# Kernel tuning notes

Hardware: AMD Instinct MI355X
Metric: run time of the kernel (lower is better)

The kernel has to match this reference:

```python
import jax, jax.numpy as jnp
import numpy as np

L, H, E, D, FF, V, CTX = 8, 16, 1024, 64, 4096, 2048, 2048
B, T = 4, 1024


def _ln(x, g, b, eps=1e-5):
    mu = x.mean(-1, keepdims=True)
    var = ((x - mu) ** 2).mean(-1, keepdims=True)
    return (x - mu) * jax.lax.rsqrt(var + eps) * g + b


def setup_inputs() -> dict:
    key = jax.random.key(0)
    ks = jax.random.split(key, 12)
    s = 0.02
    return {
        "tokens": jax.random.randint(ks[0], (B, T), 0, V),
        "tok_emb": jax.random.normal(ks[1], (V, E), jnp.float32) * s,
        "pos_emb": jax.random.normal(ks[2], (CTX, E), jnp.float32) * s,
        "Wq": jax.random.normal(ks[3], (L, H, E, D), jnp.float32) * s,
        "Wk": jax.random.normal(ks[4], (L, H, E, D), jnp.float32) * s,
        "Wv": jax.random.normal(ks[5], (L, H, E, D), jnp.float32) * s,
        "Wo": jax.random.normal(ks[6], (L, H * D, E), jnp.float32) * s,
        "bo": jnp.zeros((L, E), jnp.float32),
        "ln1_g": jnp.ones((L, E), jnp.float32),
        "ln1_b": jnp.zeros((L, E), jnp.float32),
        "ln2_g": jnp.ones((L, E), jnp.float32),
        "ln2_b": jnp.zeros((L, E), jnp.float32),
        "W1": jax.random.normal(ks[7], (L, E, FF), jnp.float32) * s,
        "b1": jnp.zeros((L, FF), jnp.float32),
        "W2": jax.random.normal(ks[8], (L, FF, E), jnp.float32) * s,
        "b2": jnp.zeros((L, E), jnp.float32),
        "lnf_g": jnp.ones((E,), jnp.float32),
        "lnf_b": jnp.zeros((E,), jnp.float32),
        "Wlm": jax.random.normal(ks[9], (E, V), jnp.float32) * s,
        "blm": jnp.zeros((V,), jnp.float32),
    }


def reference(tokens, tok_emb, pos_emb, Wq, Wk, Wv, Wo, bo, ln1_g, ln1_b,
              ln2_g, ln2_b, W1, b1, W2, b2, lnf_g, lnf_b, Wlm, blm):
    # NOTE: original indexes pos_embd with token ids (pos_embd(x.int()))
    x = tok_emb[tokens] + pos_emb[tokens]  # [B,T,E]
    t = x.shape[1]
    causal = jnp.tril(jnp.ones((t, t), bool))
    scale = 1.0 / jnp.sqrt(jnp.float32(D))
    for l in range(L):
        x = _ln(x, ln1_g[l], ln1_b[l])
        q = jnp.einsum('bte,hed->bhtd', x, Wq[l])
        k = jnp.einsum('bte,hed->bhtd', x, Wk[l])
        v = jnp.einsum('bte,hed->bhtd', x, Wv[l])
        scores = jnp.einsum('bhtd,bhsd->bhts', q, k) * scale
        scores = jnp.where(causal, scores, -jnp.inf)
        att = jax.nn.softmax(scores, axis=-1)
        o = jnp.einsum('bhts,bhsd->bhtd', att, v)
        o = o.transpose(0, 2, 1, 3).reshape(x.shape[0], t, H * D)
        x = x + o @ Wo[l] + bo[l]
        x = _ln(x, ln2_g[l], ln2_b[l])
        x = x + jax.nn.relu(x @ W1[l] + b1[l]) @ W2[l] + b2[l]
    x = _ln(x, lnf_g, lnf_b)
    return x @ Wlm + blm
```

## Files before the change

kernel.cpp:

```cpp
#include <hip/hip_runtime.h>
#include <hip/hip_bf16.h>

#define LAYERS 8
#define H_ 16
#define E_ 1024
#define D_ 64
#define FF_ 4096
#define V_ 2048
#define B_ 4
#define T_ 1024
#define MTOK (B_*T_)

typedef __bf16 bf16x8_t __attribute__((ext_vector_type(8)));
typedef __bf16 bf16x4_t __attribute__((ext_vector_type(4)));
typedef float f32x4_t __attribute__((ext_vector_type(4)));
typedef __hip_bfloat16 bf16_t;

__device__ __forceinline__ bf16_t f2b(float f) { return __float2bfloat16(f); }

__global__ void embed_kernel(const int* __restrict__ tokens,
                             const float* __restrict__ te,
                             const float* __restrict__ pe,
                             bf16_t* __restrict__ x) {
  int row = blockIdx.x;
  int tok = tokens[row];
  int t = threadIdx.x;
  float4 va = ((const float4*)(te + (size_t)tok * E_))[t];
  float4 vp = ((const float4*)(pe + (size_t)tok * E_))[t];
  bf16x4_t o;
  o[0] = (__bf16)(va.x + vp.x); o[1] = (__bf16)(va.y + vp.y);
  o[2] = (__bf16)(va.z + vp.z); o[3] = (__bf16)(va.w + vp.w);
  ((bf16x4_t*)(x + (size_t)row * E_))[t] = o;
}

__global__ __launch_bounds__(256) void ln_kernel(const bf16_t* __restrict__ xin,
                                                 bf16_t* __restrict__ xout,
                                                 const float* __restrict__ g,
                                                 const float* __restrict__ b) {
  int row = blockIdx.x, tid = threadIdx.x;
  bf16x4_t v4 = ((const bf16x4_t*)(xin + (size_t)row * E_))[tid];
  float v0 = (float)v4[0], v1 = (float)v4[1], v2 = (float)v4[2], v3 = (float)v4[3];
  float s  = v0 + v1 + v2 + v3;
  float sq = v0*v0 + v1*v1 + v2*v2 + v3*v3;
  for (int off = 32; off; off >>= 1) {
    s  += __shfl_xor(s, off, 64);
    sq += __shfl_xor(sq, off, 64);
  }
  __shared__ float2 wred[4];
  if ((tid & 63) == 0) wred[tid >> 6] = make_float2(s, sq);
  __syncthreads();
  float2 w0 = wred[0], w1 = wred[1], w2 = wred[2], w3 = wred[3];
  float S = w0.x + w1.x + w2.x + w3.x, SQ = w0.y + w1.y + w2.y + w3.y;
  float mean = S * (1.0f / E_);
  float var  = SQ * (1.0f / E_) - mean * mean;
  float inv = rsqrtf(var + 1e-5f);
  float4 gv = ((const float4*)g)[tid];
  float4 bv = ((const float4*)b)[tid];
  bf16x4_t o;
  o[0] = (__bf16)((v0 - mean) * inv * gv.x + bv.x);
  o[1] = (__bf16)((v1 - mean) * inv * gv.y + bv.y);
  o[2] = (__bf16)((v2 - mean) * inv * gv.z + bv.z);
  o[3] = (__bf16)((v3 - mean) * inv * gv.w + bv.w);
  ((bf16x4_t*)(xout + (size_t)row * E_))[tid] = o;
}

__global__ void transpose_kernel(const float* __restrict__ in, bf16_t* __restrict__ out,
                                 int R, int C) {
  __shared__ float tile[32][33];
  int z = blockIdx.z;
  const float* ib = in + (size_t)z * R * C;
  bf16_t* ob = out + (size_t)z * R * C;
  int r0 = blockIdx.y * 32, c0 = blockIdx.x * 32;
  int tx = threadIdx.x, ty = threadIdx.y;
  for (int i = 0; i < 4; i++)
    tile[ty + i * 8][tx] = ib[(size_t)(r0 + ty + i * 8) * C + (c0 + tx)];
  __syncthreads();
  for (int i = 0; i < 4; i++)
    ob[(size_t)(c0 + ty + i * 8) * R + (r0 + tx)] = f2b(tile[tx][ty + i * 8]);
}

enum { MODE_F32 = 0, MODE_BF16 = 1, MODE_QKV = 2 };

__device__ __forceinline__ void gload16(const bf16_t* g, bf16_t* l) {
  __builtin_amdgcn_global_load_lds((const __attribute__((address_space(1))) void*)g,
                                   (__attribute__((address_space(3))) void*)l, 16, 0, 0);
}

__device__ __forceinline__ int xcd_swz(int flat, int nwg) {
  int q = nwg >> 3, r = nwg & 7;
  int xcd = flat & 7, idx = flat >> 3;
  return (xcd < r ? xcd * (q + 1) : r * (q + 1) + (xcd - r) * q) + idx;
}

template <int MODE>
__global__ __launch_bounds__(512) void gemm3_kernel(
    const bf16_t* __restrict__ A, int lda,
    const bf16_t* __restrict__ Bt, int ldb,
    void* __restrict__ C, long long sCz,
    const float* __restrict__ bias,
    int M, int N, int kspan, int relu) {
  constexpr int ABUFE = 256 * 64;
  constexpr int BBUFE = 128 * 64;
  __shared__ __align__(16) bf16_t LA[3 * ABUFE];
  __shared__ __align__(16) bf16_t LB[3 * BBUFE];
  int tid = threadIdx.x, lane = tid & 63, wave = tid >> 6;
  int wm = wave >> 1, wn = wave & 1;
  int z = blockIdx.z;
  int nwg = gridDim.x * gridDim.y;
  int flat = xcd_swz(blockIdx.y * gridDim.x + blockIdx.x, nwg);
  int m0 = (flat / gridDim.x) * 256, n0 = (flat % gridDim.x) * 128;
  const bf16_t* Ab = A + (size_t)m0 * lda + (size_t)z * kspan;
  const bf16_t* Bb = Bt + (size_t)n0 * ldb + (size_t)z * kspan;
  int sr = lane & 15, sc = (lane >> 4) * 8;

  f32x4_t acc[4][4];
#pragma unroll
  for (int i = 0; i < 4; i++)
#pragma unroll
    for (int j = 0; j < 4; j++)
      acc[i][j] = (f32x4_t){0.f, 0.f, 0.f, 0.f};

  auto stageh = [&](int b, int kt, int h) {
    int kg = kt * 64;
#pragma unroll
    for (int ch = 0; ch < 2; ch++) {
      int sub = wave * 4 + 2 * h + ch;
      gload16(Ab + (size_t)((sub >> 1) * 16 + sr) * lda + kg + (sub & 1) * 32 + sc,
              LA + b * ABUFE + sub * 512);
    }
    {
      int sub = wave * 2 + h;
      gload16(Bb + (size_t)((sub >> 1) * 16 + sr) * ldb + kg + (sub & 1) * 32 + sc,
              LB + b * BBUFE + sub * 512);
    }
  };

  auto phase = [&](int b, int ks, int t, int nk) {
    bf16x8_t af[4], bfv[4];
    unsigned abase = (unsigned)(size_t)(LA + b * ABUFE);
    unsigned bbase = (unsigned)(size_t)(LB + b * BBUFE);
#pragma unroll
    for (int i = 0; i < 4; i++) {
      unsigned ad = abase + (unsigned)((((wm * 4 + i) * 2 + ks) * 512 + lane * 8) * 2);
      asm volatile("ds_read_b128 %0, %1" : "=v"(af[i]) : "v"(ad));
    }
#pragma unroll
    for (int j = 0; j < 4; j++) {
      unsigned bd = bbase + (unsigned)((((wn * 4 + j) * 2 + ks) * 512 + lane * 8) * 2);
      asm volatile("ds_read_b128 %0, %1" : "=v"(bfv[j]) : "v"(bd));
    }
    if (t + 2 < nk) stageh((t + 2) % 3, t + 2, ks);
    __builtin_amdgcn_s_barrier();
    asm volatile("s_waitcnt lgkmcnt(0)" ::: "memory");
    __builtin_amdgcn_sched_barrier(0);
    __builtin_amdgcn_s_setprio(1);
#pragma unroll
    for (int i = 0; i < 4; i++)
#pragma unroll
      for (int j = 0; j < 4; j++)
        acc[i][j] = __builtin_amdgcn_mfma_f32_16x16x32_bf16(af[i], bfv[j], acc[i][j], 0, 0, 0);
    __builtin_amdgcn_s_setprio(0);
  };

  int nk = kspan / 64;
  stageh(0, 0, 0); stageh(0, 0, 1);
  stageh(1, 1, 0); stageh(1, 1, 1);
  for (int t = 0; t < nk; ++t) {
    int b = t % 3;
    if (t + 1 < nk) { asm volatile("s_waitcnt vmcnt(6)" ::: "memory"); }
    else            { asm volatile("s_waitcnt vmcnt(0)" ::: "memory"); }
    __builtin_amdgcn_s_barrier();
    phase(b, 0, t, nk);
    phase(b, 1, t, nk);
  }

#pragma unroll
  for (int i = 0; i < 4; i++)
#pragma unroll
    for (int j = 0; j < 4; j++) {
      f32x4_t v = acc[i][j];
      int n = n0 + wn * 64 + j * 16 + (lane & 15);
      int mb = m0 + wm * 64 + i * 16 + (lane >> 4) * 4;
#pragma unroll
      for (int r = 0; r < 4; r++) {
        int m = mb + r;
        float val = v[r];
        if (bias) val += bias[n];
        if (relu) val = fmaxf(val, 0.f);
        if (MODE == MODE_F32) {
          size_t idx = (size_t)z * sCz + (size_t)m * N + n;
          ((float*)C)[idx] = val;
        } else if (MODE == MODE_BF16) {
          size_t idx = (size_t)z * sCz + (size_t)m * N + n;
          ((bf16_t*)C)[idx] = f2b(val);
        } else {
          int sect = n >> 10, hd = n & 1023, h = hd >> 6, d = hd & 63;
          int b2 = m >> 10, tt = m & 1023;
          size_t base = (size_t)sect * ((size_t)B_ * H_ * T_ * D_);
          size_t idx = base + ((size_t)(b2 * H_ + h) << 16) +
                       (sect == 2 ? (size_t)((d << 10) + tt) : (size_t)((tt << 6) + d));
          ((bf16_t*)C)[idx] = f2b(val);
        }
      }
    }
}

template <int NS>
__global__ __launch_bounds__(256) void splitk_reduce_kernel(const bf16_t* __restrict__ p,
                                                            const bf16_t* __restrict__ t,
                                                            bf16_t* __restrict__ r,
                                                            const float* __restrict__ bias) {
  size_t i = (size_t)blockIdx.x * 256 + threadIdx.x;
  bf16x8_t tv = ((const bf16x8_t*)t)[i];
  int base = (int)((i * 8) & (E_ - 1));
  float acc[8];
#pragma unroll
  for (int j = 0; j < 8; j++) acc[j] = (float)tv[j] + bias[base + j];
#pragma unroll
  for (int s = 0; s < NS; s++) {
    bf16x8_t pv = ((const bf16x8_t*)p)[i + (size_t)s * ((size_t)MTOK * E_ / 8)];
#pragma unroll
    for (int j = 0; j < 8; j++) acc[j] += (float)pv[j];
  }
  bf16x8_t ov;
#pragma unroll
  for (int j = 0; j < 8; j++) ov[j] = (__bf16)acc[j];
  ((bf16x8_t*)r)[i] = ov;
}

#define KPAD 72

__global__ __launch_bounds__(256) void flash_kernel(
    const bf16_t* __restrict__ q,
    const bf16_t* __restrict__ kk,
    const bf16_t* __restrict__ vt,
    bf16_t* __restrict__ o) {
  __shared__ __align__(16) bf16_t Ks[64 * KPAD];
  __shared__ __align__(16) bf16_t Vs[64 * KPAD];
  __shared__ __align__(16) bf16_t Ps[4][16 * KPAD];
  int bid = blockIdx.x;
  int qi = 15 - (bid >> 6);
  int bh = bid & 63;
  int b = bh >> 4, h = bh & 15;
  const bf16_t* qb = q + ((size_t)bh << 16);
  const bf16_t* kb = kk + ((size_t)bh << 16);
  const bf16_t* vb = vt + ((size_t)bh << 16);
  int tid = threadIdx.x, lane = tid & 63, wave = tid >> 6;
  int lr = lane & 15, lg = lane >> 4;
  int qbase = qi * 64;

  bf16x8_t qf[2];
  {
    const bf16_t* qrow = qb + (size_t)(qbase + wave * 16 + lr) * D_ + lg * 8;
    qf[0] = *(const bf16x8_t*)(qrow);
    qf[1] = *(const bf16x8_t*)(qrow + 32);
  }

  float m_r[4], l_r[4];
  f32x4_t oc[4];
#pragma unroll
  for (int r = 0; r < 4; r++) { m_r[r] = -1e30f; l_r[r] = 0.f; }
#pragma unroll
  for (int j = 0; j < 4; j++) oc[j] = (f32x4_t){0.f, 0.f, 0.f, 0.f};

  int srow = tid >> 2, scol = (tid & 3) * 16;

  bf16x8_t k0, k1, v0, v1;
  {
    const bf16_t* kg = kb + (size_t)srow * D_ + scol;
    k0 = *(const bf16x8_t*)kg;
    k1 = *(const bf16x8_t*)(kg + 8);
    const bf16_t* vg = vb + (size_t)srow * T_ + scol;
    v0 = *(const bf16x8_t*)vg;
    v1 = *(const bf16x8_t*)(vg + 8);
  }

  for (int s = 0; s <= qi; s++) {
    __syncthreads();
    *(bf16x8_t*)(&Ks[srow * KPAD + scol]) = k0;
    *(bf16x8_t*)(&Ks[srow * KPAD + scol + 8]) = k1;
    *(bf16x8_t*)(&Vs[srow * KPAD + scol]) = v0;
    *(bf16x8_t*)(&Vs[srow * KPAD + scol + 8]) = v1;
    __syncthreads();

    if (s < qi) {
      int kv1 = (s + 1) * 64;
      const bf16_t* kg = kb + (size_t)(kv1 + srow) * D_ + scol;
      k0 = *(const bf16x8_t*)kg;
      k1 = *(const bf16x8_t*)(kg + 8);
      const bf16_t* vg = vb + (size_t)srow * T_ + kv1 + scol;
      v0 = *(const bf16x8_t*)vg;
      v1 = *(const bf16x8_t*)(vg + 8);
    }

    int kv0 = s * 64;
    f32x4_t sc[4];
#pragma unroll
    for (int j = 0; j < 4; j++) {
      f32x4_t a = (f32x4_t){0.f, 0.f, 0.f, 0.f};
      bf16x8_t b0 = *(const bf16x8_t*)(&Ks[(j * 16 + lr) * KPAD + lg * 8]);
      bf16x8_t b1 = *(const bf16x8_t*)(&Ks[(j * 16 + lr) * KPAD + lg * 8 + 32]);
      a = __builtin_amdgcn_mfma_f32_16x16x32_bf16(qf[0], b0, a, 0, 0, 0);
      a = __builtin_amdgcn_mfma_f32_16x16x32_bf16(qf[1], b1, a, 0, 0, 0);
      sc[j] = a;
    }
    if (s == qi) {
#pragma unroll
      for (int j = 0; j < 4; j++)
#pragma unroll
        for (int r = 0; r < 4; r++) {
          int kvp = kv0 + j * 16 + lr;
          int qp  = qbase + wave * 16 + lg * 4 + r;
          sc[j][r] = (kvp <= qp) ? sc[j][r] * 0.125f : -1e30f;
        }
    } else {
#pragma unroll
      for (int j = 0; j < 4; j++)
#pragma unroll
        for (int r = 0; r < 4; r++) sc[j][r] *= 0.125f;
    }

    float ex[4];
#pragma unroll
    for (int r = 0; r < 4; r++) {
      float v = fmaxf(fmaxf(sc[0][r], sc[1][r]), fmaxf(sc[2][r], sc[3][r]));
      v = fmaxf(v, __shfl_xor(v, 1, 64));
      v = fmaxf(v, __shfl_xor(v, 2, 64));
      v = fmaxf(v, __shfl_xor(v, 4, 64));
      v = fmaxf(v, __shfl_xor(v, 8, 64));
      float mn = fmaxf(m_r[r], v);
      ex[r] = __expf(m_r[r] - mn);
      m_r[r] = mn;
      l_r[r] *= ex[r];
    }
#pragma unroll
    for (int j = 0; j < 4; j++)
#pragma unroll
      for (int r = 0; r < 4; r++) {
        float p = __expf(sc[j][r] - m_r[r]);
        l_r[r] += p;
        Ps[wave][(lg * 4 + r) * KPAD + j * 16 + lr] = f2b(p);
      }

#pragma unroll
    for (int j = 0; j < 4; j++)
#pragma unroll
      for (int r = 0; r < 4; r++) oc[j][r] *= ex[r];

    bf16x8_t pa0 = *(const bf16x8_t*)(&Ps[wave][lr * KPAD + lg * 8]);
    bf16x8_t pa1 = *(const bf16x8_t*)(&Ps[wave][lr * KPAD + lg * 8 + 32]);
#pragma unroll
    for (int j = 0; j < 4; j++) {
      bf16x8_t vb0 = *(const bf16x8_t*)(&Vs[(j * 16 + lr) * KPAD + lg * 8]);
      bf16x8_t vb1 = *(const bf16x8_t*)(&Vs[(j * 16 + lr) * KPAD + lg * 8 + 32]);
      oc[j] = __builtin_amdgcn_mfma_f32_16x16x32_bf16(pa0, vb0, oc[j], 0, 0, 0);
      oc[j] = __builtin_amdgcn_mfma_f32_16x16x32_bf16(pa1, vb1, oc[j], 0, 0, 0);
    }
  }

#pragma unroll
  for (int r = 0; r < 4; r++) {
    float v = l_r[r];
    v += __shfl_xor(v, 1, 64);
    v += __shfl_xor(v, 2, 64);
    v += __shfl_xor(v, 4, 64);
    v += __shfl_xor(v, 8, 64);
    l_r[r] = 1.f / v;
  }
  bf16_t* ob = o + ((size_t)(b * T_ + qbase + wave * 16)) * (H_ * D_) + h * D_;
#pragma unroll
  for (int j = 0; j < 4; j++)
#pragma unroll
    for (int r = 0; r < 4; r++) {
      int qrow = lg * 4 + r;
      ob[(size_t)qrow * (H_ * D_) + j * 16 + lr] = f2b(oc[j][r] * l_r[r]);
    }
}

extern "C" void kernel_launch(void* const* d_in, const int* in_sizes, int n_in,
                              void* d_out, int out_size, void* d_ws, size_t ws_size,
                              hipStream_t stream) {
  (void)in_sizes; (void)n_in; (void)out_size; (void)ws_size;
  const int*   tokens = (const int*)d_in[0];
  const float* tok_emb = (const float*)d_in[1];
  const float* pos_emb = (const float*)d_in[2];
  const float* Wq = (const float*)d_in[3];
  const float* Wk = (const float*)d_in[4];
  const float* Wv = (const float*)d_in[5];
  const float* Wo = (const float*)d_in[6];
  const float* bo = (const float*)d_in[7];
  const float* ln1_g = (const float*)d_in[8];
  const float* ln1_b = (const float*)d_in[9];
  const float* ln2_g = (const float*)d_in[10];
  const float* ln2_b = (const float*)d_in[11];
  const float* W1 = (const float*)d_in[12];
  const float* b1 = (const float*)d_in[13];
  const float* W2 = (const float*)d_in[14];
  const float* b2 = (const float*)d_in[15];
  const float* lnf_g = (const float*)d_in[16];
  const float* lnf_b = (const float*)d_in[17];
  const float* Wlm = (const float*)d_in[18];
  const float* blm = (const float*)d_in[19];

  char* w = (char*)d_ws;
  size_t off = 0;
  auto alloc = [&](size_t bytes) { void* p = (void*)(w + off); off += (bytes + 255) & ~(size_t)255; return p; };
  bf16_t* r    = (bf16_t*)alloc((size_t)MTOK * E_ * 2);
  bf16_t* t    = (bf16_t*)alloc((size_t)MTOK * E_ * 2);
  bf16_t* q    = (bf16_t*)alloc((size_t)B_ * H_ * T_ * D_ * 2);
  bf16_t* kk   = (bf16_t*)alloc((size_t)B_ * H_ * T_ * D_ * 2);
  bf16_t* vt   = (bf16_t*)alloc((size_t)B_ * H_ * T_ * D_ * 2);
  bf16_t* o    = (bf16_t*)alloc((size_t)MTOK * E_ * 2);
  bf16_t* h1   = (bf16_t*)alloc((size_t)MTOK * FF_ * 2);
  bf16_t* WqkvT = (bf16_t*)alloc((size_t)3 * E_ * H_ * D_ * 2);
  bf16_t* WoT  = (bf16_t*)alloc((size_t)E_ * H_ * D_ * 2);
  bf16_t* W1T  = (bf16_t*)alloc((size_t)E_ * FF_ * 2);
  bf16_t* W2T  = (bf16_t*)alloc((size_t)E_ * FF_ * 2);
  bf16_t* WlmT = (bf16_t*)alloc((size_t)E_ * V_ * 2);
  bf16_t* p2   = (bf16_t*)alloc((size_t)2 * MTOK * E_ * 2);

  embed_kernel<<<MTOK, 256, 0, stream>>>(tokens, tok_emb, pos_emb, r);
  transpose_kernel<<<dim3(V_ / 32, E_ / 32, 1), dim3(32, 8), 0, stream>>>(Wlm, WlmT, E_, V_);

  for (int l = 0; l < LAYERS; l++) {
    ln_kernel<<<MTOK, 256, 0, stream>>>(r, t, ln1_g + l * E_, ln1_b + l * E_);

    transpose_kernel<<<dim3(D_ / 32, E_ / 32, H_), dim3(32, 8), 0, stream>>>(
        Wq + (size_t)l * H_ * E_ * D_, WqkvT, E_, D_);
    transpose_kernel<<<dim3(D_ / 32, E_ / 32, H_), dim3(32, 8), 0, stream>>>(
        Wk + (size_t)l * H_ * E_ * D_, WqkvT + (size_t)E_ * H_ * D_, E_, D_);
    transpose_kernel<<<dim3(D_ / 32, E_ / 32, H_), dim3(32, 8), 0, stream>>>(
        Wv + (size_t)l * H_ * E_ * D_, WqkvT + (size_t)2 * E_ * H_ * D_, E_, D_);
    transpose_kernel<<<dim3(E_ / 32, (H_ * D_) / 32, 1), dim3(32, 8), 0, stream>>>(
        Wo + (size_t)l * H_ * D_ * E_, WoT, H_ * D_, E_);
    transpose_kernel<<<dim3(FF_ / 32, E_ / 32, 1), dim3(32, 8), 0, stream>>>(
        W1 + (size_t)l * E_ * FF_, W1T, E_, FF_);
    transpose_kernel<<<dim3(E_ / 32, FF_ / 32, 1), dim3(32, 8), 0, stream>>>(
        W2 + (size_t)l * FF_ * E_, W2T, FF_, E_);

    gemm3_kernel<MODE_QKV><<<dim3(24, 16, 1), 512, 0, stream>>>(
        t, E_, WqkvT, E_, q, 0, nullptr, MTOK, 3 * H_ * D_, E_, 0);

    flash_kernel<<<1024, 256, 0, stream>>>(q, kk, vt, o);

    gemm3_kernel<MODE_BF16><<<dim3(8, 16, 2), 512, 0, stream>>>(
        o, H_ * D_, WoT, H_ * D_, p2, (long long)MTOK * E_, nullptr,
        MTOK, E_, (H_ * D_) / 2, 0);
    splitk_reduce_kernel<2><<<MTOK * E_ / 2048, 256, 0, stream>>>(p2, t, r, bo + l * E_);

    ln_kernel<<<MTOK, 256, 0, stream>>>(r, t, ln2_g + l * E_, ln2_b + l * E_);

    gemm3_kernel<MODE_BF16><<<dim3(32, 16, 1), 512, 0, stream>>>(
        t, E_, W1T, E_, h1, 0, b1 + l * FF_, MTOK, FF_, E_, 1);
    gemm3_kernel<MODE_BF16><<<dim3(8, 16, 2), 512, 0, stream>>>(
        h1, FF_, W2T, FF_, p2, (long long)MTOK * E_, nullptr, MTOK, E_, FF_ / 2, 0);
    splitk_reduce_kernel<2><<<MTOK * E_ / 2048, 256, 0, stream>>>(p2, t, r, b2 + l * E_);
  }

  ln_kernel<<<MTOK, 256, 0, stream>>>(r, t, lnf_g, lnf_b);
  gemm3_kernel<MODE_F32><<<dim3(16, 16, 1), 512, 0, stream>>>(
      t, E_, WlmT, E_, d_out, 0, blm, MTOK, V_, E_, 0);
}
```

Before: 2.277 ms.

## Fuse split-K reduce with LayerNorm, merge weight transposes, add smaller-tile GEMM

Replaces the FFN split-K reduce plus the next layer's LayerNorm with one kernel that writes both the residual and the normalized activations. All per-layer weight transposes now run in a single launch. The QKV and output-projection GEMMs move to a new 256-thread, 128x128, double-buffered GEMM, and the output projection folds bias and residual into its epilogue instead of using split-K. This removes several launches and full-activation round trips, but the new GEMM has smaller tiles and may be less efficient than the 3-stage one.

Measured after the change: 2.115 ms. 1.08x faster.

```diff
diff --git a/kernel.cpp b/kernel.cpp
--- a/kernel.cpp
+++ b/kernel.cpp
@@ -64,22 +64,106 @@
   ((bf16x4_t*)(xout + (size_t)row * E_))[tid] = o;
 }
 
+__global__ __launch_bounds__(256) void reduce_ln_kernel(
+    const bf16_t* __restrict__ p,
+    const bf16_t* __restrict__ tin,
+    const float* __restrict__ bias,
+    bf16_t* __restrict__ r,
+    bf16_t* __restrict__ tout,
+    const float* __restrict__ g,
+    const float* __restrict__ b) {
+  int row = blockIdx.x, tid = threadIdx.x;
+  size_t base = (size_t)row * E_ + tid * 4;
+  bf16x4_t tv = *(const bf16x4_t*)(tin + base);
+  bf16x4_t p0 = *(const bf16x4_t*)(p + base);
+  bf16x4_t p1 = *(const bf16x4_t*)(p + (size_t)MTOK * E_ + base);
+  float4 bv = ((const float4*)bias)[tid];
+  float y0 = (float)tv[0] + (float)p0[0] + (float)p1[0] + bv.x;
+  float y1 = (float)tv[1] + (float)p0[1] + (float)p1[1] + bv.y;
+  float y2 = (float)tv[2] + (float)p0[2] + (float)p1[2] + bv.z;
+  float y3 = (float)tv[3] + (float)p0[3] + (float)p1[3] + bv.w;
+  bf16x4_t rv;
+  rv[0] = (__bf16)y0; rv[1] = (__bf16)y1; rv[2] = (__bf16)y2; rv[3] = (__bf16)y3;
+  *(bf16x4_t*)(r + base) = rv;
+  float z0 = (float)rv[0], z1 = (float)rv[1], z2 = (float)rv[2], z3 = (float)rv[3];
+  float s = z0 + z1 + z2 + z3, sq = z0*z0 + z1*z1 + z2*z2 + z3*z3;
+  for (int off = 32; off; off >>= 1) {
+    s  += __shfl_xor(s, off, 64);
+    sq += __shfl_xor(sq, off, 64);
+  }
+  __shared__ float2 wred[4];
+  if ((tid & 63) == 0) wred[tid >> 6] = make_float2(s, sq);
+  __syncthreads();
+  float2 w0 = wred[0], w1 = wred[1], w2 = wred[2], w3 = wred[3];
+  float S = w0.x + w1.x + w2.x + w3.x, SQ = w0.y + w1.y + w2.y + w3.y;
+  float mean = S * (1.0f / E_);
+  float var  = SQ * (1.0f / E_) - mean * mean;
+  float inv = rsqrtf(var + 1e-5f);
+  float4 gv = ((const float4*)g)[tid];
+  float4 b2v = ((const float4*)b)[tid];
+  bf16x4_t o;
+  o[0] = (__bf16)((z0 - mean) * inv * gv.x + b2v.x);
+  o[1] = (__bf16)((z1 - mean) * inv * gv.y + b2v.y);
+  o[2] = (__bf16)((z2 - mean) * inv * gv.z + b2v.z);
+  o[3] = (__bf16)((z3 - mean) * inv * gv.w + b2v.w);
+  *(bf16x4_t*)(tout + base) = o;
+}
+
+__global__ void prep_weights_kernel(const float* __restrict__ Wq,
+                                    const float* __restrict__ Wk,
+                                    const float* __restrict__ Wv,
+                                    const float* __restrict__ Wo,
+                                    const float* __restrict__ W1,
+                                    const float* __restrict__ W2,
+                                    bf16_t* __restrict__ WqkvT,
+                                    bf16_t* __restrict__ WoT,
+                                    bf16_t* __restrict__ W1T,
+                                    bf16_t* __restrict__ W2T,
+                                    int l) {
+  __shared__ float tile[32][33];
+  int bid = blockIdx.x;
+  const float* src; bf16_t* dst; int R, C, r0, c0;
+  if (bid < 3072) {
+    int op = bid >> 10, rem = bid & 1023;
+    int h = rem >> 6, tt = rem & 63;
+    const float* W = (op == 0) ? Wq : (op == 1) ? Wk : Wv;
+    src = W + (size_t)l * H_ * E_ * D_ + (size_t)h * E_ * D_;
+    dst = WqkvT + (size_t)op * E_ * H_ * D_ + (size_t)h * E_ * D_;
+    R = E_; C = D_; r0 = (tt >> 1) * 32; c0 = (tt & 1) * 32;
+  } else if (bid < 4096) {
+    int tt = bid - 3072;
+    src = Wo + (size_t)l * H_ * D_ * E_; dst = WoT;
+    R = H_ * D_; C = E_; r0 = (tt >> 5) * 32; c0 = (tt & 31) * 32;
+  } else if (bid < 8192) {
+    int tt = bid - 4096;
+    src = W1 + (size_t)l * E_ * FF_; dst = W1T;
+    R = E_; C = FF_; r0 = (tt >> 7) * 32; c0 = (tt & 127) * 32;
+  } else {
+    int tt = bid - 8192;
+    src = W2 + (size_t)l * FF_ * E_; dst = W2T;
+    R = FF_; C = E_; r0 = (tt >> 5) * 32; c0 = (tt & 31) * 32;
+  }
+  int tx = threadIdx.x, ty = threadIdx.y;
+  for (int i = 0; i < 4; i++)
+    tile[ty + i * 8][tx] = src[(size_t)(r0 + ty + i * 8) * C + (c0 + tx)];
+  __syncthreads();
+  for (int i = 0; i < 4; i++)
+    dst[(size_t)(c0 + ty + i * 8) * R + (r0 + tx)] = f2b(tile[tx][ty + i * 8]);
+}
+
 __global__ void transpose_kernel(const float* __restrict__ in, bf16_t* __restrict__ out,
                                  int R, int C) {
   __shared__ float tile[32][33];
-  int z = blockIdx.z;
-  const float* ib = in + (size_t)z * R * C;
-  bf16_t* ob = out + (size_t)z * R * C;
   int r0 = blockIdx.y * 32, c0 = blockIdx.x * 32;
   int tx = threadIdx.x, ty = threadIdx.y;
   for (int i = 0; i < 4; i++)
-    tile[ty + i * 8][tx] = ib[(size_t)(r0 + ty + i * 8) * C + (c0 + tx)];
+    tile[ty + i * 8][tx] = in[(size_t)(r0 + ty + i * 8) * C + (c0 + tx)];
   __syncthreads();
   for (int i = 0; i < 4; i++)
-    ob[(size_t)(c0 + ty + i * 8) * R + (r0 + tx)] = f2b(tile[tx][ty + i * 8]);
-}
-
-enum { MODE_F32 = 0, MODE_BF16 = 1, MODE_QKV = 2 };
+    out[(size_t)(c0 + ty + i * 8) * R + (r0 + tx)] = f2b(tile[tx][ty + i * 8]);
+}
+
+enum { MODE_F32 = 0, MODE_BF16 = 1, MODE_QKV = 2, MODE_BF16R = 3 };
 
 __device__ __forceinline__ void gload16(const bf16_t* g, bf16_t* l) {
   __builtin_amdgcn_global_load_lds((const __attribute__((address_space(1))) void*)g,
@@ -90,6 +174,103 @@
   int q = nwg >> 3, r = nwg & 7;
   int xcd = flat & 7, idx = flat >> 3;
   return (xcd < r ? xcd * (q + 1) : r * (q + 1) + (xcd - r) * q) + idx;
+}
+
+#define BK 32
+template <int BM, int BN, int MODE>
+__global__ __launch_bounds__(256) void gemm97_kernel(
+    const bf16_t* __restrict__ A, long long sAz, int lda,
+    const bf16_t* __restrict__ Bt, long long sBz, int ldb,
+    void* __restrict__ C, long long sCz,
+    const float* __restrict__ bias,
+    const void* __restrict__ resid,
+    int M, int N, int K, int relu) {
+  constexpr int FR = BM / 32, FC = BN / 32;
+  constexpr int A_ISS = BM / 64, B_ISS = BN / 64;
+  __shared__ __align__(16) bf16_t As[2][BM * BK];
+  __shared__ __align__(16) bf16_t Bs[2][BN * BK];
+  int tid = threadIdx.x;
+  int z = blockIdx.z;
+  int nwg = gridDim.x * gridDim.y;
+  int flat = xcd_swz(blockIdx.y * gridDim.x + blockIdx.x, nwg);
+  int m0 = (flat / gridDim.x) * BM, n0 = (flat % gridDim.x) * BN;
+  const bf16_t* Ab = A + (size_t)z * sAz + (size_t)m0 * lda;
+  const bf16_t* Bb = Bt + (size_t)z * sBz + (size_t)n0 * ldb;
+  int lane = tid & 63, wave = tid >> 6;
+  int wr = (wave >> 1) * (BM / 2), wc = (wave & 1) * (BN / 2);
+  int lr = lane & 15, lk = (lane >> 4) * 8;
+  int srow = tid >> 2;
+  int scol = (tid & 3) * 8;
+
+  f32x4_t acc[FR][FC];
+  for (int i = 0; i < FR; i++)
+    for (int j = 0; j < FC; j++)
+      acc[i][j] = (f32x4_t){0.f, 0.f, 0.f, 0.f};
+
+  auto stage = [&](int buf, int k0) {
+#pragma unroll
+    for (int i = 0; i < A_ISS; i++)
+      gload16(Ab + (size_t)(i * 64 + srow) * lda + k0 + scol, &As[buf][i * 2048 + wave * 512]);
+#pragma unroll
+    for (int i = 0; i < B_ISS; i++)
+      gload16(Bb + (size_t)(i * 64 + srow) * ldb + k0 + scol, &Bs[buf][i * 2048 + wave * 512]);
+  };
+
+  int nk = K / BK;
+  stage(0, 0);
+  __syncthreads();
+  int cur = 0;
+  for (int kt = 0; kt < nk; ++kt) {
+    if (kt + 1 < nk) stage(cur ^ 1, (kt + 1) * BK);
+    bf16x8_t af[FR], bfv[FC];
+#pragma unroll
+    for (int i = 0; i < FR; i++)
+      af[i] = *(const bf16x8_t*)(&As[cur][(wr + i * 16 + lr) * BK + lk]);
+#pragma unroll
+    for (int j = 0; j < FC; j++)
+      bfv[j] = *(const bf16x8_t*)(&Bs[cur][(wc + j * 16 + lr) * BK + lk]);
+#pragma unroll
+    for (int i = 0; i < FR; i++)
+#pragma unroll
+      for (int j = 0; j < FC; j++)
+        acc[i][j] = __builtin_amdgcn_mfma_f32_16x16x32_bf16(af[i], bfv[j], acc[i][j], 0, 0, 0);
+    __syncthreads();
+    cur ^= 1;
+  }
+
+#pragma unroll
+  for (int i = 0; i < FR; i++)
+#pragma unroll
+    for (int j = 0; j < FC; j++) {
+      f32x4_t v = acc[i][j];
+      int n = n0 + wc + j * 16 + lr;
+      int mb = m0 + wr + i * 16 + (lane >> 4) * 4;
+#pragma unroll
+      for (int r = 0; r < 4; r++) {
+        int m = mb + r;
+        float val = v[r];
+        if (bias) val += bias[n];
+        if (relu) val = fmaxf(val, 0.f);
+        if (MODE == MODE_F32) {
+          size_t idx = (size_t)z * sCz + (size_t)m * N + n;
+          ((float*)C)[idx] = val;
+        } else if (MODE == MODE_BF16) {
+          size_t idx = (size_t)z * sCz + (size_t)m * N + n;
+          ((bf16_t*)C)[idx] = f2b(val);
+        } else if (MODE == MODE_BF16R) {
+          size_t idx = (size_t)m * N + n;
+          val += __bfloat162float(((const bf16_t*)resid)[idx]);
+          ((bf16_t*)C)[idx] = f2b(val);
+        } else {
+          int sect = n >> 10, hd = n & 1023, h = hd >> 6, d = hd & 63;
+          int b = m >> 10, t = m & 1023;
+          size_t base = (size_t)sect * ((size_t)B_ * H_ * T_ * D_);
+          size_t idx = base + ((size_t)(b * H_ + h) << 16) +
+                       (sect == 2 ? (size_t)((d << 10) + t) : (size_t)((t << 6) + d));
+          ((bf16_t*)C)[idx] = f2b(val);
+        }
+      }
+    }
 }
 
 template <int MODE>
@@ -190,42 +371,12 @@
         if (MODE == MODE_F32) {
           size_t idx = (size_t)z * sCz + (size_t)m * N + n;
           ((float*)C)[idx] = val;
-        } else if (MODE == MODE_BF16) {
+        } else {
           size_t idx = (size_t)z * sCz + (size_t)m * N + n;
-          ((bf16_t*)C)[idx] = f2b(val);
-        } else {
-          int sect = n >> 10, hd = n & 1023, h = hd >> 6, d = hd & 63;
-          int b2 = m >> 10, tt = m & 1023;
-          size_t base = (size_t)sect * ((size_t)B_ * H_ * T_ * D_);
-          size_t idx = base + ((size_t)(b2 * H_ + h) << 16) +
-                       (sect == 2 ? (size_t)((d << 10) + tt) : (size_t)((tt << 6) + d));
           ((bf16_t*)C)[idx] = f2b(val);
         }
       }
     }
-}
-
-template <int NS>
-__global__ __launch_bounds__(256) void splitk_reduce_kernel(const bf16_t* __restrict__ p,
-                                                            const bf16_t* __restrict__ t,
-                                                            bf16_t* __restrict__ r,
-                                                            const float* __restrict__ bias) {
-  size_t i = (size_t)blockIdx.x * 256 + threadIdx.x;
-  bf16x8_t tv = ((const bf16x8_t*)t)[i];
-  int base = (int)((i * 8) & (E_ - 1));
-  float acc[8];
-#pragma unroll
-  for (int j = 0; j < 8; j++) acc[j] = (float)tv[j] + bias[base + j];
-#pragma unroll
-  for (int s = 0; s < NS; s++) {
-    bf16x8_t pv = ((const bf16x8_t*)p)[i + (size_t)s * ((size_t)MTOK * E_ / 8)];
-#pragma unroll
-    for (int j = 0; j < 8; j++) acc[j] += (float)pv[j];
-  }
-  bf16x8_t ov;
-#pragma unroll
-  for (int j = 0; j < 8; j++) ov[j] = (__bf16)acc[j];
-  ((bf16x8_t*)r)[i] = ov;
 }
 
 #define KPAD 72
@@ -420,33 +571,20 @@
   bf16_t* p2   = (bf16_t*)alloc((size_t)2 * MTOK * E_ * 2);
 
   embed_kernel<<<MTOK, 256, 0, stream>>>(tokens, tok_emb, pos_emb, r);
-  transpose_kernel<<<dim3(V_ / 32, E_ / 32, 1), dim3(32, 8), 0, stream>>>(Wlm, WlmT, E_, V_);
+  transpose_kernel<<<dim3(V_ / 32, E_ / 32), dim3(32, 8), 0, stream>>>(Wlm, WlmT, E_, V_);
+  ln_kernel<<<MTOK, 256, 0, stream>>>(r, t, ln1_g, ln1_b);
 
   for (int l = 0; l < LAYERS; l++) {
-    ln_kernel<<<MTOK, 256, 0, stream>>>(r, t, ln1_g + l * E_, ln1_b + l * E_);
-
-    transpose_kernel<<<dim3(D_ / 32, E_ / 32, H_), dim3(32, 8), 0, stream>>>(
-        Wq + (size_t)l * H_ * E_ * D_, WqkvT, E_, D_);
-    transpose_kernel<<<dim3(D_ / 32, E_ / 32, H_), dim3(32, 8), 0, stream>>>(
-        Wk + (size_t)l * H_ * E_ * D_, WqkvT + (size_t)E_ * H_ * D_, E_, D_);
-    transpose_kernel<<<dim3(D_ / 32, E_ / 32, H_), dim3(32, 8), 0, stream>>>(
-        Wv + (size_t)l * H_ * E_ * D_, WqkvT + (size_t)2 * E_ * H_ * D_, E_, D_);
-    transpose_kernel<<<dim3(E_ / 32, (H_ * D_) / 32, 1), dim3(32, 8), 0, stream>>>(
-        Wo + (size_t)l * H_ * D_ * E_, WoT, H_ * D_, E_);
-    transpose_kernel<<<dim3(FF_ / 32, E_ / 32, 1), dim3(32, 8), 0, stream>>>(
-        W1 + (size_t)l * E_ * FF_, W1T, E_, FF_);
-    transpose_kernel<<<dim3(E_ / 32, FF_ / 32, 1), dim3(32, 8), 0, stream>>>(
-        W2 + (size_t)l * FF_ * E_, W2T, FF_, E_);
-
-    gemm3_kernel<MODE_QKV><<<dim3(24, 16, 1), 512, 0, stream>>>(
-        t, E_, WqkvT, E_, q, 0, nullptr, MTOK, 3 * H_ * D_, E_, 0);
+    prep_weights_kernel<<<12288, dim3(32, 8), 0, stream>>>(
+        Wq, Wk, Wv, Wo, W1, W2, WqkvT, WoT, W1T, W2T, l);
+
+    gemm97_kernel<128, 128, MODE_QKV><<<dim3(24, 32, 1), 256, 0, stream>>>(
+        t, 0, E_, WqkvT, 0, E_, q, 0, nullptr, nullptr, MTOK, 3 * H_ * D_, E_, 0);
 
     flash_kernel<<<1024, 256, 0, stream>>>(q, kk, vt, o);
 
-    gemm3_kernel<MODE_BF16><<<dim3(8, 16, 2), 512, 0, stream>>>(
-        o, H_ * D_, WoT, H_ * D_, p2, (long long)MTOK * E_, nullptr,
-        MTOK, E_, (H_ * D_) / 2, 0);
-    splitk_reduce_kernel<2><<<MTOK * E_ / 2048, 256, 0, stream>>>(p2, t, r, bo + l * E_);
+    gemm97_kernel<128, 128, MODE_BF16R><<<dim3(8, 32, 1), 256, 0, stream>>>(
+        o, 0, H_ * D_, WoT, 0, H_ * D_, r, 0, bo + l * E_, t, MTOK, E_, H_ * D_, 0);
 
     ln_kernel<<<MTOK, 256, 0, stream>>>(r, t, ln2_g + l * E_, ln2_b + l * E_);
 
@@ -454,10 +592,11 @@
         t, E_, W1T, E_, h1, 0, b1 + l * FF_, MTOK, FF_, E_, 1);
     gemm3_kernel<MODE_BF16><<<dim3(8, 16, 2), 512, 0, stream>>>(
         h1, FF_, W2T, FF_, p2, (long long)MTOK * E_, nullptr, MTOK, E_, FF_ / 2, 0);
-    splitk_reduce_kernel<2><<<MTOK * E_ / 2048, 256, 0, stream>>>(p2, t, r, b2 + l * E_);
-  }
-
-  ln_kernel<<<MTOK, 256, 0, stream>>>(r, t, lnf_g, lnf_b);
+    const float* gn = (l + 1 < LAYERS) ? (ln1_g + (l + 1) * E_) : lnf_g;
+    const float* bn = (l + 1 < LAYERS) ? (ln1_b + (l + 1) * E_) : lnf_b;
+    reduce_ln_kernel<<<MTOK, 256, 0, stream>>>(p2, t, b2 + l * E_, r, t, gn, bn);
+  }
+
   gemm3_kernel<MODE_F32><<<dim3(16, 16, 1), 512, 0, stream>>>(
       t, E_, WlmT, E_, d_out, 0, blm, MTOK, V_, E_, 0);
 }
```
